# Performance work log

Measured on AMD Instinct MI355X. Metric: run time of the kernel, lower is better.

## Reference

```python
import jax, jax.numpy as jnp
import numpy as np

NT = 128          # num_timesteps (reference query points)
E = 128           # embed_time
H = 128           # nhidden
NH = 1            # num_heads
F = 32            # feature_size
NS = 2            # num_states
EPS = 1e-5


def layer_norm(x, g, b):
    m = jnp.mean(x, axis=-1, keepdims=True)
    v = jnp.mean((x - m) ** 2, axis=-1, keepdims=True)
    return (x - m) * jax.lax.rsqrt(v + EPS) * g + b


def setup_inputs() -> dict:
    key = jax.random.key(0)
    ks = jax.random.split(key, 24)
    nrm = lambda k, s: (jax.random.normal(k, s) * 0.05).astype(jnp.float32)
    inp = {
        "input": jax.random.normal(ks[0], (8, F, 512), dtype=jnp.float32),
        "mask": jax.random.randint(ks[1], (8, F, 512), 0, 2).astype(jnp.float32),
        "timesteps": jnp.sort(jax.random.uniform(ks[2], (8, 512), dtype=jnp.float32), axis=-1),
        # time embedding
        "periodic_w": nrm(ks[3], (E - 1, 1)), "periodic_b": nrm(ks[4], (E - 1,)),
        "lin_w": nrm(ks[5], (1, 1)), "lin_b": nrm(ks[6], (1,)),
        # query / key projections + layer norms
        "q_w": nrm(ks[7], (E, E)), "q_b": nrm(ks[8], (E,)),
        "q_g": jnp.ones((E,), jnp.float32), "q_be": jnp.zeros((E,), jnp.float32),
        "k_w": nrm(ks[9], (E, E)), "k_b": nrm(ks[10], (E,)),
        "k_g": jnp.ones((E,), jnp.float32), "k_be": jnp.zeros((E,), jnp.float32),
        # attention_norm over h*2F channels, then output linear + LN to nhidden
        "attn_g": jnp.ones((NH * 2 * F,), jnp.float32), "attn_b": jnp.zeros((NH * 2 * F,), jnp.float32),
        "out_w": nrm(ks[11], (H, NH * 2 * F)), "out_b": nrm(ks[12], (H,)),
        "out_g": jnp.ones((H,), jnp.float32), "out_be": jnp.zeros((H,), jnp.float32),
        # GRU (torch gate order r, z, n)
        "gru_wih": nrm(ks[13], (3 * H, H)), "gru_whh": nrm(ks[14], (3 * H, H)),
        "gru_bih": nrm(ks[15], (3 * H,)), "gru_bhh": nrm(ks[16], (3 * H,)),
        # classifier MLP
        "c1_w": nrm(ks[17], (H, H)), "c1_b": nrm(ks[18], (H,)),
        "c2_w": nrm(ks[19], (H, H)), "c2_b": nrm(ks[20], (H,)),
        "c3_w": nrm(ks[21], (NS, H)), "c3_b": nrm(ks[22], (NS,)),
    }
    return inp


def time_embedding(tt, lin_w, lin_b, periodic_w, periodic_b):
    t = tt[..., None]                                   # (..., 1)
    out1 = t @ lin_w.T + lin_b                          # (..., 1)
    out2 = jnp.sin(t @ periodic_w.T + periodic_b)       # (..., E-1)
    return jnp.concatenate([out1, out2], axis=-1)       # (..., E)


def reference(input, mask, timesteps, periodic_w, periodic_b, lin_w, lin_b,
              q_w, q_b, q_g, q_be, k_w, k_b, k_g, k_be,
              attn_g, attn_b, out_w, out_b, out_g, out_be,
              gru_wih, gru_whh, gru_bih, gru_bhh,
              c1_w, c1_b, c2_w, c2_b, c3_w, c3_b):
    B = input.shape[0]
    x_in = jnp.transpose(input, (0, 2, 1))              # (B, T, F)
    m = 1.0 - jnp.transpose(mask, (0, 2, 1))            # (B, T, F)
    x_in = x_in * (m > 0).astype(x_in.dtype)
    x = jnp.concatenate([x_in, m], axis=-1)             # (B, T, 2F)
    mk = jnp.concatenate([m, m], axis=-1)               # (B, T, 2F)

    key_e = time_embedding(timesteps, lin_w, lin_b, periodic_w, periodic_b)        # (B, T, E)
    qtimes = jnp.linspace(0.0, 1.0, NT)
    query_e = time_embedding(qtimes[None], lin_w, lin_b, periodic_w, periodic_b)   # (1, NT, E)

    q = layer_norm(query_e @ q_w.T + q_b, q_g, q_be)    # (1, NT, E)
    k = layer_norm(key_e @ k_w.T + k_b, k_g, k_be)      # (B, T, E)

    etk = E // NH
    q = q.reshape(1, NT, NH, etk).transpose(0, 2, 1, 3)         # (1, h, NT, etk)
    k = k.reshape(B, -1, NH, etk).transpose(0, 2, 1, 3)         # (B, h, T, etk)

    scores = jnp.einsum("ahqd,bhkd->bhqk", q, k) / np.sqrt(etk)  # (B, h, NT, T)
    # per-channel masked softmax over keys: (B, h, NT, T, 2F)
    logits = jnp.where(mk[:, None, None, :, :] == 0, -1e9, scores[..., None])
    p_attn = jax.nn.softmax(logits, axis=-2)
    att = jnp.sum(p_attn * x[:, None, None, :, :], axis=-2)     # (B, h, NT, 2F)

    x2 = att.transpose(0, 2, 1, 3).reshape(B, NT, NH * 2 * F)
    x2 = layer_norm(x2, attn_g, attn_b)
    out = layer_norm(x2 @ out_w.T + out_b, out_g, out_be)       # (B, NT, H)

    # GRU over the NT reference timesteps, last hidden state
    seq = out.transpose(1, 0, 2)                                # (NT, B, H)
    h0 = jnp.zeros((B, H), out.dtype)

    def gru_step(h, x_t):
        gi = x_t @ gru_wih.T + gru_bih
        gh = h @ gru_whh.T + gru_bhh
        ir, iz, inn = jnp.split(gi, 3, axis=-1)
        hr, hz, hn = jnp.split(gh, 3, axis=-1)
        r = jax.nn.sigmoid(ir + hr)
        z = jax.nn.sigmoid(iz + hz)
        n = jnp.tanh(inn + r * hn)
        h_new = (1.0 - z) * n + z * h
        return h_new, None

    h_last, _ = jax.lax.scan(gru_step, h0, seq)

    h1 = jax.nn.relu(h_last @ c1_w.T + c1_b)
    h2 = jax.nn.relu(h1 @ c2_w.T + c2_b)
    return h2 @ c3_w.T + c3_b                                   # (B, num_states) logits
```

## Files before the change

kernel.cpp:

```cpp
#include <hip/hip_runtime.h>
#include <math.h>

#define LN_EPS 1e-5f

typedef _Float16 h2v __attribute__((ext_vector_type(2)));

__device__ __forceinline__ float dot4(float4 a, float4 b) {
    return a.x*b.x + a.y*b.y + a.z*b.z + a.w*b.w;
}
__device__ __forceinline__ void fma4(float4& a, float s, float4 v) {
    a.x += s*v.x; a.y += s*v.y; a.z += s*v.z; a.w += s*v.w;
}
__device__ __forceinline__ float fast_rcp(float x) {
    return __builtin_amdgcn_rcpf(x);
}
__device__ __forceinline__ float fast_sigmoid(float x) {
    return fast_rcp(1.f + __expf(-x));
}
__device__ __forceinline__ float fast_tanh(float x) {
    return 1.f - 2.f*fast_rcp(__expf(2.f*x) + 1.f);
}
__device__ __forceinline__ float fdot2u(unsigned int a, unsigned int b, float c) {
#if __has_builtin(__builtin_amdgcn_fdot2)
    return __builtin_amdgcn_fdot2(__builtin_bit_cast(h2v, a),
                                  __builtin_bit_cast(h2v, b), c, false);
#else
    const h2v av = __builtin_bit_cast(h2v, a);
    const h2v bv = __builtin_bit_cast(h2v, b);
    return c + (float)av[0]*(float)bv[0] + (float)av[1]*(float)bv[1];
#endif
}
__device__ __forceinline__ float wsum64(float v) {
    #pragma unroll
    for (int off = 32; off > 0; off >>= 1) v += __shfl_xor(v, off);
    return v;
}

__global__ void k_embed_proj(
    const float* __restrict__ input, const float* __restrict__ mask,
    const float* __restrict__ timesteps,
    const float* __restrict__ pw, const float* __restrict__ pb,
    const float* __restrict__ lw, const float* __restrict__ lb,
    const float* __restrict__ q_w, const float* __restrict__ q_b,
    const float* __restrict__ q_g, const float* __restrict__ q_be,
    const float* __restrict__ k_w, const float* __restrict__ k_b,
    const float* __restrict__ k_g, const float* __restrict__ k_be,
    float* __restrict__ qs, float* __restrict__ kT, float2* __restrict__ xm)
{
    const int blk = blockIdx.x;
    const int tid = threadIdx.x;

    __shared__ __align__(16) float e[4][128];
    __shared__ __align__(16) float4 red[128];
    __shared__ __align__(16) float proj[4][128];
    __shared__ __align__(16) float2 tile[32][65];

    if (blk < 64) {
        const int b  = blk >> 3;
        const int t0 = (blk & 7) * 64;
        const int cg = tid >> 6;
        const int tt = tid & 63;
        #pragma unroll
        for (int c16 = 0; c16 < 16; ++c16) {
            const int c = c16*2 + cg;
            const float m = mask [(size_t)(b*32 + c)*512 + t0 + tt];
            const float x = input[(size_t)(b*32 + c)*512 + t0 + tt];
            const float mm = 1.0f - m;
            tile[c][tt] = make_float2(x*mm, mm);
        }
        __syncthreads();
        const int c2 = tid & 31;
        const int tg = tid >> 5;
        #pragma unroll
        for (int k = 0; k < 16; ++k) {
            const int t = tg*16 + k;
            xm[((size_t)b*512 + t0 + t)*32 + c2] = tile[c2][t];
        }
        return;
    }

    const bool isq = blk < 96;
    float tv[4];
    int kidx0 = 0;
    if (isq) {
        const int q0 = (blk - 64) * 4;
        #pragma unroll
        for (int r = 0; r < 4; ++r) tv[r] = (float)(q0 + r) * (1.0f/127.0f);
    } else {
        kidx0 = (blk - 96) * 4;
        #pragma unroll
        for (int r = 0; r < 4; ++r) tv[r] = timesteps[kidx0 + r];
    }

    float pwj = 0.f, pbj = 0.f;
    if (tid > 0) { pwj = pw[tid-1]; pbj = pb[tid-1]; }
    const float lw0 = lw[0], lb0 = lb[0];
    #pragma unroll
    for (int r = 0; r < 4; ++r)
        e[r][tid] = (tid == 0) ? (tv[r]*lw0 + lb0) : sinf(tv[r]*pwj + pbj);
    __syncthreads();

    const float* W  = isq ? q_w  : k_w;
    const float* Bv = isq ? q_b  : k_b;
    const float* G  = isq ? q_g  : k_g;
    const float* Be = isq ? q_be : k_be;

    {
        const int jj = tid >> 2, dc = tid & 3;
        const float4* e0 = (const float4*)(&e[0][0]);
        const float4* e1 = (const float4*)(&e[1][0]);
        const float4* e2 = (const float4*)(&e[2][0]);
        const float4* e3 = (const float4*)(&e[3][0]);
        #pragma unroll
        for (int jb = 0; jb < 4; ++jb) {
            const int j = jb*32 + jj;
            const float4* wrow = (const float4*)(W + (size_t)j*128);
            float a0=0.f, a1=0.f, a2=0.f, a3=0.f;
            #pragma unroll
            for (int k = 0; k < 8; ++k) {
                const int idx = dc + 4*k;
                const float4 w4 = wrow[idx];
                a0 += dot4(w4, e0[idx]);
                a1 += dot4(w4, e1[idx]);
                a2 += dot4(w4, e2[idx]);
                a3 += dot4(w4, e3[idx]);
            }
            a0 += __shfl_xor(a0, 1, 4); a0 += __shfl_xor(a0, 2, 4);
            a1 += __shfl_xor(a1, 1, 4); a1 += __shfl_xor(a1, 2, 4);
            a2 += __shfl_xor(a2, 1, 4); a2 += __shfl_xor(a2, 2, 4);
            a3 += __shfl_xor(a3, 1, 4); a3 += __shfl_xor(a3, 2, 4);
            if (dc == 0) {
                const float bj = Bv[j];
                proj[0][j] = a0 + bj; proj[1][j] = a1 + bj;
                proj[2][j] = a2 + bj; proj[3][j] = a3 + bj;
            }
        }
    }
    __syncthreads();

    float acc[4];
    #pragma unroll
    for (int r = 0; r < 4; ++r) acc[r] = proj[r][tid];

    red[tid] = make_float4(acc[0], acc[1], acc[2], acc[3]);
    __syncthreads();
    for (int s = 64; s > 0; s >>= 1) {
        if (tid < s) {
            float4 m = red[tid]; const float4 o = red[tid+s];
            m.x += o.x; m.y += o.y; m.z += o.z; m.w += o.w;
            red[tid] = m;
        }
        __syncthreads();
    }
    float4 mean = red[0];
    mean.x *= (1.0f/128.0f); mean.y *= (1.0f/128.0f);
    mean.z *= (1.0f/128.0f); mean.w *= (1.0f/128.0f);
    __syncthreads();
    const float d0 = acc[0]-mean.x, d1 = acc[1]-mean.y,
                d2 = acc[2]-mean.z, d3 = acc[3]-mean.w;
    red[tid] = make_float4(d0*d0, d1*d1, d2*d2, d3*d3);
    __syncthreads();
    for (int s = 64; s > 0; s >>= 1) {
        if (tid < s) {
            float4 m = red[tid]; const float4 o = red[tid+s];
            m.x += o.x; m.y += o.y; m.z += o.z; m.w += o.w;
            red[tid] = m;
        }
        __syncthreads();
    }
    float4 var = red[0];
    var.x *= (1.0f/128.0f); var.y *= (1.0f/128.0f);
    var.z *= (1.0f/128.0f); var.w *= (1.0f/128.0f);

    const float gg = G[tid], bb = Be[tid];
    const float o0 = d0*rsqrtf(var.x+LN_EPS)*gg + bb;
    const float o1 = d1*rsqrtf(var.y+LN_EPS)*gg + bb;
    const float o2 = d2*rsqrtf(var.z+LN_EPS)*gg + bb;
    const float o3 = d3*rsqrtf(var.w+LN_EPS)*gg + bb;

    if (isq) {
        const float sc = 0.08838834764831845f;
        const int q0 = (blk - 64)*4;
        qs[(size_t)(q0+0)*128 + tid] = o0*sc;
        qs[(size_t)(q0+1)*128 + tid] = o1*sc;
        qs[(size_t)(q0+2)*128 + tid] = o2*sc;
        qs[(size_t)(q0+3)*128 + tid] = o3*sc;
    } else {
        const int b = kidx0 >> 9;
        const int t = kidx0 & 511;
        *(float4*)(kT + ((size_t)(b*128 + tid))*512 + t) =
            make_float4(o0, o1, o2, o3);
    }
}

__global__ void __launch_bounds__(256) k_attn(
    const float2* __restrict__ xm,
    const float* __restrict__ qs, const float* __restrict__ kT,
    const float* __restrict__ attn_g, const float* __restrict__ attn_b,
    const float* __restrict__ out_w, const float* __restrict__ out_b,
    const float* __restrict__ out_g, const float* __restrict__ out_be,
    float* __restrict__ outm)
{
    const int b     = blockIdx.x >> 5;
    const int qbase = (blockIdx.x & 31) * 4;
    const int tid   = threadIdx.x;

    __shared__ __align__(16) float et[4][512];
    __shared__ __align__(16) float qsh[4][128];
    __shared__ __align__(16) float wsh[128*66];
    __shared__ __align__(16) float sA[4][8][32];
    __shared__ __align__(16) float aA[4][8][32];
    __shared__ __align__(16) float x2s[4][64];
    __shared__ float redC[4];

    for (int idx = tid; idx < 512; idx += 256)
        qsh[idx >> 7][idx & 127] = qs[(size_t)(qbase + (idx >> 7))*128 + (idx & 127)];
    for (int idx = tid; idx < 8192; idx += 256)
        wsh[(idx >> 6)*66 + (idx & 63)] = out_w[idx];
    __syncthreads();

    {
        const int grp = tid >> 7;
        const int tl  = tid & 127;
        const int q0  = grp*2;
        const float4* kp  = (const float4*)kT + (size_t)b*128*128 + tl;
        const float4* qa4 = (const float4*)qsh[q0];
        const float4* qb4 = (const float4*)qsh[q0+1];
        float4 a0 = make_float4(0,0,0,0), a1 = make_float4(0,0,0,0);
        float4 c0 = kp[0], c1 = kp[128], c2 = kp[256], c3 = kp[384];
        for (int c = 0; c < 32; ++c) {
            float4 n0, n1, n2, n3;
            if (c < 31) {
                const float4* kn = kp + (size_t)(4*c+4)*128;
                n0 = kn[0]; n1 = kn[128]; n2 = kn[256]; n3 = kn[384];
            }
            const float4 qa = qa4[c], qb = qb4[c];
            fma4(a0, qa.x, c0); fma4(a1, qb.x, c0);
            fma4(a0, qa.y, c1); fma4(a1, qb.y, c1);
            fma4(a0, qa.z, c2); fma4(a1, qb.z, c2);
            fma4(a0, qa.w, c3); fma4(a1, qb.w, c3);
            c0 = n0; c1 = n1; c2 = n2; c3 = n3;
        }
        a0.x = __expf(a0.x); a0.y = __expf(a0.y); a0.z = __expf(a0.z); a0.w = __expf(a0.w);
        a1.x = __expf(a1.x); a1.y = __expf(a1.y); a1.z = __expf(a1.z); a1.w = __expf(a1.w);
        ((float4*)et[q0])[tl]   = a0;
        ((float4*)et[q0+1])[tl] = a1;
    }
    __syncthreads();

    {
        const int c   = tid & 31;
        const int seg = tid >> 5;
        const float2* xp = xm + ((size_t)b*512 + seg*64)*32 + c;
        float s0=0,s1=0,s2=0,s3=0, a0=0,a1=0,a2=0,a3=0;
        #pragma unroll 4
        for (int i = 0; i < 64; ++i) {
            const float2 v = xp[(size_t)i*32];
            const int t = seg*64 + i;
            const float w0 = et[0][t]*v.y, w1 = et[1][t]*v.y;
            const float w2 = et[2][t]*v.y, w3 = et[3][t]*v.y;
            s0 += w0; s1 += w1; s2 += w2; s3 += w3;
            a0 += w0*v.x; a1 += w1*v.x; a2 += w2*v.x; a3 += w3*v.x;
        }
        sA[0][seg][c]=s0; sA[1][seg][c]=s1; sA[2][seg][c]=s2; sA[3][seg][c]=s3;
        aA[0][seg][c]=a0; aA[1][seg][c]=a1; aA[2][seg][c]=a2; aA[3][seg][c]=a3;
    }
    __syncthreads();

    {
        const int ql = tid >> 6;
        const int c2 = tid & 63;
        const int cc = c2 & 31;
        float ss = 0.f;
        #pragma unroll
        for (int g = 0; g < 8; ++g) ss += sA[ql][g][cc];
        float attv;
        if (c2 < 32) {
            float aa = 0.f;
            #pragma unroll
            for (int g = 0; g < 8; ++g) aa += aA[ql][g][cc];
            attv = (ss > 0.f) ? aa/ss : 0.f;
        } else {
            attv = (ss > 0.f) ? 1.0f : 0.0f;
        }
        const float mean = wsum64(attv) * (1.0f/64.0f);
        const float dv = attv - mean;
        const float var = wsum64(dv*dv) * (1.0f/64.0f);
        x2s[ql][c2] = dv*rsqrtf(var+LN_EPS)*attn_g[c2] + attn_b[c2];
    }
    __syncthreads();

    {
        const int jhalf = tid >> 7;
        const int j     = tid & 127;
        const int wave  = tid >> 6;
        for (int lq2 = 0; lq2 < 2; ++lq2) {
            const int ql = jhalf*2 + lq2;
            float acc = out_b[j];
            const float4* wrow = (const float4*)(wsh + j*66);
            const float4* xr   = (const float4*)x2s[ql];
            #pragma unroll
            for (int k = 0; k < 16; ++k) acc += dot4(wrow[k], xr[k]);

            float v = wsum64(acc);
            if ((tid & 63) == 0) redC[wave] = v;
            __syncthreads();
            const float mean = (redC[jhalf*2] + redC[jhalf*2+1]) * (1.0f/128.0f);
            __syncthreads();
            const float d = acc - mean;
            v = wsum64(d*d);
            if ((tid & 63) == 0) redC[wave] = v;
            __syncthreads();
            const float var = (redC[jhalf*2] + redC[jhalf*2+1]) * (1.0f/128.0f);
            outm[((size_t)b*128 + qbase + ql)*128 + j] =
                d*rsqrtf(var+LN_EPS)*out_g[j] + out_be[j];
            __syncthreads();
        }
    }
}

__global__ void k_gi(const float* __restrict__ outm,
                     const float* __restrict__ wih, const float* __restrict__ bih,
                     float* __restrict__ gi)
{
    const int qi  = blockIdx.x;
    const int tid = threadIdx.x;
    __shared__ __align__(16) float rows[8][128];
    for (int idx = tid; idx < 1024; idx += 384) {
        const int b = idx >> 7, d = idx & 127;
        rows[b][d] = outm[(size_t)(b*128+qi)*128 + d];
    }
    __syncthreads();

    const int g0 = tid >> 2, dc = tid & 3;
    #pragma unroll
    for (int gb = 0; gb < 4; ++gb) {
        const int g = gb*96 + g0;
        const float4* wrow = (const float4*)(wih + (size_t)g*128);
        float acc[8] = {0,0,0,0,0,0,0,0};
        #pragma unroll
        for (int k = 0; k < 8; ++k) {
            const int idx = dc + 4*k;
            const float4 w4 = wrow[idx];
            #pragma unroll
            for (int b = 0; b < 8; ++b)
                acc[b] += dot4(w4, ((const float4*)rows[b])[idx]);
        }
        #pragma unroll
        for (int b = 0; b < 8; ++b) {
            acc[b] += __shfl_xor(acc[b], 1, 4);
            acc[b] += __shfl_xor(acc[b], 2, 4);
        }
        if (dc == 0) {
            const float bi = bih[g];
            #pragma unroll
            for (int b = 0; b < 8; ++b)
                gi[((size_t)qi*8 + b)*384 + g] = acc[b] + bi;
        }
    }
}

__global__ void __launch_bounds__(512) k_gru_cls(
    const float* __restrict__ gi,
    const float* __restrict__ whh, const float* __restrict__ bhh,
    const float* __restrict__ c1w, const float* __restrict__ c1b,
    const float* __restrict__ c2w, const float* __restrict__ c2b,
    const float* __restrict__ c3w, const float* __restrict__ c3b,
    float* __restrict__ out)
{
    const int b   = blockIdx.x;
    const int tid = threadIdx.x;
    const int s   = tid >> 7;
    const int u   = tid & 127;

    __shared__ __align__(16) unsigned int lds[25344];
    unsigned int* hP = lds;
    float4* part4 = (float4*)&lds[64];
    float* hcls = (float*)&lds[64 + 1536];

    {
        const float4* w4 = (const float4*)whh;
        #pragma unroll 4
        for (int k = 0; k < 24; ++k) {
            const int idx = tid + k*512;
            const float4 v = w4[idx];
            const int row = idx >> 5, c4 = idx & 31;
            h2v p0; p0[0] = (_Float16)v.x; p0[1] = (_Float16)v.y;
            h2v p1; p1[0] = (_Float16)v.z; p1[1] = (_Float16)v.w;
            lds[row*66 + c4*2    ] = __builtin_bit_cast(unsigned int, p0);
            lds[row*66 + c4*2 + 1] = __builtin_bit_cast(unsigned int, p1);
        }
    }
    __syncthreads();

    unsigned int wreg[3][16];
    #pragma unroll
    for (int g = 0; g < 3; ++g) {
        const uint2* src = (const uint2*)&lds[(g*128 + u)*66 + 16*s];
        #pragma unroll
        for (int i = 0; i < 8; ++i) {
            const uint2 t = src[i];
            wreg[g][2*i] = t.x; wreg[g][2*i+1] = t.y;
        }
    }
    __syncthreads();

    const float* gbase = gi + (size_t)b*384;
    float bh_r=0.f, bh_z=0.f, bh_n=0.f, gr0=0.f, gz0=0.f, gn0=0.f, hprev=0.f;
    if (tid < 64) hP[tid] = 0u;
    if (s == 0) {
        bh_r = bhh[u]; bh_z = bhh[u+128]; bh_n = bhh[u+256];
        gr0 = gbase[u]; gz0 = gbase[u+128]; gn0 = gbase[u+256];
    }
    __syncthreads();

    for (int qi = 0; qi < 128; ++qi) {
        const uint4* hp4 = (const uint4*)hP + s*4;
        float ar = 0.f, az = 0.f, an = 0.f;
        #pragma unroll
        for (int i = 0; i < 4; ++i) {
            const uint4 hv = hp4[i];
            ar = fdot2u(wreg[0][4*i+0], hv.x, ar);
            ar = fdot2u(wreg[0][4*i+1], hv.y, ar);
            ar = fdot2u(wreg[0][4*i+2], hv.z, ar);
            ar = fdot2u(wreg[0][4*i+3], hv.w, ar);
            az = fdot2u(wreg[1][4*i+0], hv.x, az);
            az = fdot2u(wreg[1][4*i+1], hv.y, az);
            az = fdot2u(wreg[1][4*i+2], hv.z, az);
            az = fdot2u(wreg[1][4*i+3], hv.w, az);
            an = fdot2u(wreg[2][4*i+0], hv.x, an);
            an = fdot2u(wreg[2][4*i+1], hv.y, an);
            an = fdot2u(wreg[2][4*i+2], hv.z, an);
            an = fdot2u(wreg[2][4*i+3], hv.w, an);
        }
        if (s > 0) part4[(s-1)*128 + u] = make_float4(ar, az, an, 0.f);

        float grn=0.f, gzn=0.f, gnn=0.f;
        if (s == 0 && qi < 127) {
            const float* gb = gbase + (size_t)(qi+1)*3072;
            grn = gb[u]; gzn = gb[u+128]; gnn = gb[u+256];
        }
        __syncthreads();

        if (s == 0) {
            const float4 p0 = part4[u], p1 = part4[128+u], p2 = part4[256+u];
            const float ghr = ar + p0.x + p1.x + p2.x + bh_r;
            const float ghz = az + p0.y + p1.y + p2.y + bh_z;
            const float ghn = an + p0.z + p1.z + p2.z + bh_n;
            const float r = fast_sigmoid(gr0 + ghr);
            const float z = fast_sigmoid(gz0 + ghz);
            const float n = fast_tanh(gn0 + r*ghn);
            const float hn2 = (1.f - z)*n + z*hprev;
            hprev = hn2;
            gr0 = grn; gz0 = gzn; gn0 = gnn;
            const float other = __shfl_xor(hn2, 1);
            if ((u & 1) == 0) {
                h2v hp; hp[0] = (_Float16)hn2; hp[1] = (_Float16)other;
                hP[u >> 1] = __builtin_bit_cast(unsigned int, hp);
            }
        }
        __syncthreads();
    }

    float* scr = (float*)part4;
    if (s == 0) hcls[u] = hprev;
    __syncthreads();
    if (tid < 128) {
        float acc = c1b[u];
        const float4* wc = (const float4*)(c1w + (size_t)u*128);
        const float4* v  = (const float4*)hcls;
        #pragma unroll
        for (int d4 = 0; d4 < 32; ++d4) acc += dot4(wc[d4], v[d4]);
        scr[u] = fmaxf(acc, 0.f);
    }
    __syncthreads();
    if (tid < 128) {
        float acc = c2b[u];
        const float4* wc = (const float4*)(c2w + (size_t)u*128);
        const float4* v  = (const float4*)scr;
        #pragma unroll
        for (int d4 = 0; d4 < 32; ++d4) acc += dot4(wc[d4], v[d4]);
        scr[128 + u] = fmaxf(acc, 0.f);
    }
    __syncthreads();
    if (tid < 2) {
        float acc = c3b[tid];
        const float4* wc = (const float4*)(c3w + (size_t)tid*128);
        const float4* v  = (const float4*)(scr + 128);
        #pragma unroll
        for (int d4 = 0; d4 < 32; ++d4) acc += dot4(wc[d4], v[d4]);
        out[(size_t)b*2 + tid] = acc;
    }
}

extern "C" void kernel_launch(void* const* d_in, const int* in_sizes, int n_in,
                              void* d_out, int out_size, void* d_ws, size_t ws_size,
                              hipStream_t stream)
{
    const float* input     = (const float*)d_in[0];
    const float* mask      = (const float*)d_in[1];
    const float* timesteps = (const float*)d_in[2];
    const float* pw        = (const float*)d_in[3];
    const float* pb        = (const float*)d_in[4];
    const float* lw        = (const float*)d_in[5];
    const float* lb        = (const float*)d_in[6];
    const float* q_w       = (const float*)d_in[7];
    const float* q_b       = (const float*)d_in[8];
    const float* q_g       = (const float*)d_in[9];
    const float* q_be      = (const float*)d_in[10];
    const float* k_w       = (const float*)d_in[11];
    const float* k_b       = (const float*)d_in[12];
    const float* k_g       = (const float*)d_in[13];
    const float* k_be      = (const float*)d_in[14];
    const float* attn_g    = (const float*)d_in[15];
    const float* attn_b    = (const float*)d_in[16];
    const float* out_w     = (const float*)d_in[17];
    const float* out_b     = (const float*)d_in[18];
    const float* out_g     = (const float*)d_in[19];
    const float* out_be    = (const float*)d_in[20];
    const float* gru_wih   = (const float*)d_in[21];
    const float* gru_whh   = (const float*)d_in[22];
    const float* gru_bih   = (const float*)d_in[23];
    const float* gru_bhh   = (const float*)d_in[24];
    const float* c1_w      = (const float*)d_in[25];
    const float* c1_b      = (const float*)d_in[26];
    const float* c2_w      = (const float*)d_in[27];
    const float* c2_b      = (const float*)d_in[28];
    const float* c3_w      = (const float*)d_in[29];
    const float* c3_b      = (const float*)d_in[30];

    float* ws   = (float*)d_ws;
    float*  qs   = ws;
    float*  kT   = qs   + 16384;
    float*  outm = kT   + 524288;
    float*  gi   = outm + 131072;
    float2* xm   = (float2*)(gi + 393216);

    k_embed_proj<<<1120, 128, 0, stream>>>(input, mask, timesteps,
                                           pw, pb, lw, lb,
                                           q_w, q_b, q_g, q_be,
                                           k_w, k_b, k_g, k_be, qs, kT, xm);
    k_attn<<<256, 256, 0, stream>>>(xm, qs, kT,
                                    attn_g, attn_b, out_w, out_b,
                                    out_g, out_be, outm);
    k_gi<<<128, 384, 0, stream>>>(outm, gru_wih, gru_bih, gi);
    k_gru_cls<<<8, 512, 0, stream>>>(gi, gru_whh, gru_bhh,
                                     c1_w, c1_b, c2_w, c2_b, c3_w, c3_b,
                                     (float*)d_out);
}
```

Baseline: 240.5 us.

## Fuse all stages into one cooperative persistent kernel with grid syncs

Replaces the four separate kernel launches (embedding/projection, attention, GRU input projection, GRU+classifier) with a single cooperative kernel of 256 blocks of 512 threads. Grid-wide syncs separate the phases, and work items are remapped onto the persistent blocks. The outm buffer appears to be dropped, suggesting attention output now feeds the gi computation more directly. This removes launch gaps and inter-kernel drain, at the cost of grid sync overhead and a large shared-memory footprint per block.

```diff
diff --git a/kernel.cpp b/kernel.cpp
--- a/kernel.cpp
+++ b/kernel.cpp
@@ -1,5 +1,8 @@
 #include <hip/hip_runtime.h>
+#include <hip/hip_cooperative_groups.h>
 #include <math.h>
+
+namespace cg = cooperative_groups;
 
 #define LN_EPS 1e-5f
 
@@ -36,460 +39,461 @@
     return v;
 }
 
-__global__ void k_embed_proj(
-    const float* __restrict__ input, const float* __restrict__ mask,
-    const float* __restrict__ timesteps,
-    const float* __restrict__ pw, const float* __restrict__ pb,
-    const float* __restrict__ lw, const float* __restrict__ lb,
-    const float* __restrict__ q_w, const float* __restrict__ q_b,
-    const float* __restrict__ q_g, const float* __restrict__ q_be,
-    const float* __restrict__ k_w, const float* __restrict__ k_b,
-    const float* __restrict__ k_g, const float* __restrict__ k_be,
-    float* __restrict__ qs, float* __restrict__ kT, float2* __restrict__ xm)
+struct KP {
+    const float *input, *mask, *timesteps, *pw, *pb, *lw, *lb;
+    const float *q_w, *q_b, *q_g, *q_be, *k_w, *k_b, *k_g, *k_be;
+    const float *attn_g, *attn_b, *out_w, *out_b, *out_g, *out_be;
+    const float *wih, *whh, *bih, *bhh;
+    const float *c1w, *c1b, *c2w, *c2b, *c3w, *c3b;
+    float *qs, *kT, *gi;
+    float2 *xm;
+    float *out;
+};
+
+__global__ void __launch_bounds__(512) k_fused(KP p)
 {
+    __shared__ __align__(16) unsigned int lds[25344];
     const int blk = blockIdx.x;
     const int tid = threadIdx.x;
-
-    __shared__ __align__(16) float e[4][128];
-    __shared__ __align__(16) float4 red[128];
-    __shared__ __align__(16) float proj[4][128];
-    __shared__ __align__(16) float2 tile[32][65];
-
-    if (blk < 64) {
-        const int b  = blk >> 3;
-        const int t0 = (blk & 7) * 64;
-        const int cg = tid >> 6;
-        const int tt = tid & 63;
-        #pragma unroll
-        for (int c16 = 0; c16 < 16; ++c16) {
-            const int c = c16*2 + cg;
-            const float m = mask [(size_t)(b*32 + c)*512 + t0 + tt];
-            const float x = input[(size_t)(b*32 + c)*512 + t0 + tt];
-            const float mm = 1.0f - m;
-            tile[c][tt] = make_float2(x*mm, mm);
-        }
-        __syncthreads();
-        const int c2 = tid & 31;
-        const int tg = tid >> 5;
-        #pragma unroll
-        for (int k = 0; k < 16; ++k) {
-            const int t = tg*16 + k;
-            xm[((size_t)b*512 + t0 + t)*32 + c2] = tile[c2][t];
-        }
-        return;
+    cg::grid_group grid = cg::this_grid();
+
+    {
+        const int sg = tid >> 7;
+        const int t1 = tid & 127;
+        float*  e_    = (float*)lds;
+        float4* red4  = (float4*)((char*)lds + 8192);
+        float*  proj_ = (float*)((char*)lds + 16384);
+        float2* tile  = (float2*)lds;
+
+        for (int u = blk; u < 280; u += 256) {
+            if (u < 264) {
+                const bool isq = (u >= 256);
+                const int base = (isq ? (u - 256) : u) * 16 + sg * 4;
+                float tv[4];
+                #pragma unroll
+                for (int r = 0; r < 4; ++r)
+                    tv[r] = isq ? (float)(base + r) * (1.0f/127.0f)
+                                : p.timesteps[base + r];
+                float pwj = 0.f, pbj = 0.f;
+                if (t1 > 0) { pwj = p.pw[t1-1]; pbj = p.pb[t1-1]; }
+                const float lw0 = p.lw[0], lb0 = p.lb[0];
+                #pragma unroll
+                for (int r = 0; r < 4; ++r)
+                    e_[(sg*4 + r)*128 + t1] =
+                        (t1 == 0) ? (tv[r]*lw0 + lb0) : sinf(tv[r]*pwj + pbj);
+                __syncthreads();
+
+                const float* W  = isq ? p.q_w  : p.k_w;
+                const float* Bv = isq ? p.q_b  : p.k_b;
+                const float* G  = isq ? p.q_g  : p.k_g;
+                const float* Be = isq ? p.q_be : p.k_be;
+
+                {
+                    const int jj = t1 >> 2, dc = t1 & 3;
+                    const float4* e0 = (const float4*)(e_ + (sg*4+0)*128);
+                    const float4* e1 = (const float4*)(e_ + (sg*4+1)*128);
+                    const float4* e2 = (const float4*)(e_ + (sg*4+2)*128);
+                    const float4* e3 = (const float4*)(e_ + (sg*4+3)*128);
+                    #pragma unroll
+                    for (int jb = 0; jb < 4; ++jb) {
+                        const int j = jb*32 + jj;
+                        const float4* wrow = (const float4*)(W + (size_t)j*128);
+                        float a0=0.f, a1=0.f, a2=0.f, a3=0.f;
+                        #pragma unroll
+                        for (int k = 0; k < 8; ++k) {
+                            const int idx = dc + 4*k;
+                            const float4 w4 = wrow[idx];
+                            a0 += dot4(w4, e0[idx]);
+                            a1 += dot4(w4, e1[idx]);
+                            a2 += dot4(w4, e2[idx]);
+                            a3 += dot4(w4, e3[idx]);
+                        }
+                        a0 += __shfl_xor(a0, 1, 4); a0 += __shfl_xor(a0, 2, 4);
+                        a1 += __shfl_xor(a1, 1, 4); a1 += __shfl_xor(a1, 2, 4);
+                        a2 += __shfl_xor(a2, 1, 4); a2 += __shfl_xor(a2, 2, 4);
+                        a3 += __shfl_xor(a3, 1, 4); a3 += __shfl_xor(a3, 2, 4);
+                        if (dc == 0) {
+                            const float bj = Bv[j];
+                            proj_[(sg*4+0)*128 + j] = a0 + bj;
+                            proj_[(sg*4+1)*128 + j] = a1 + bj;
+                            proj_[(sg*4+2)*128 + j] = a2 + bj;
+                            proj_[(sg*4+3)*128 + j] = a3 + bj;
+                        }
+                    }
+                }
+                __syncthreads();
+
+                float acc[4];
+                #pragma unroll
+                for (int r = 0; r < 4; ++r) acc[r] = proj_[(sg*4+r)*128 + t1];
+
+                red4[sg*128 + t1] = make_float4(acc[0], acc[1], acc[2], acc[3]);
+                __syncthreads();
+                for (int s = 64; s > 0; s >>= 1) {
+                    if (t1 < s) {
+                        float4 m = red4[sg*128 + t1];
+                        const float4 o = red4[sg*128 + t1 + s];
+                        m.x += o.x; m.y += o.y; m.z += o.z; m.w += o.w;
+                        red4[sg*128 + t1] = m;
+                    }
+                    __syncthreads();
+                }
+                float4 mean = red4[sg*128];
+                mean.x *= (1.0f/128.0f); mean.y *= (1.0f/128.0f);
+                mean.z *= (1.0f/128.0f); mean.w *= (1.0f/128.0f);
+                __syncthreads();
+                const float d0 = acc[0]-mean.x, d1 = acc[1]-mean.y,
+                            d2 = acc[2]-mean.z, d3 = acc[3]-mean.w;
+                red4[sg*128 + t1] = make_float4(d0*d0, d1*d1, d2*d2, d3*d3);
+                __syncthreads();
+                for (int s = 64; s > 0; s >>= 1) {
+                    if (t1 < s) {
+                        float4 m = red4[sg*128 + t1];
+                        const float4 o = red4[sg*128 + t1 + s];
+                        m.x += o.x; m.y += o.y; m.z += o.z; m.w += o.w;
+                        red4[sg*128 + t1] = m;
+                    }
+                    __syncthreads();
+                }
+                float4 var = red4[sg*128];
+                var.x *= (1.0f/128.0f); var.y *= (1.0f/128.0f);
+                var.z *= (1.0f/128.0f); var.w *= (1.0f/128.0f);
+
+                const float gg = G[t1], bb = Be[t1];
+                const float o0 = d0*rsqrtf(var.x+LN_EPS)*gg + bb;
+                const float o1 = d1*rsqrtf(var.y+LN_EPS)*gg + bb;
+                const float o2 = d2*rsqrtf(var.z+LN_EPS)*gg + bb;
+                const float o3 = d3*rsqrtf(var.w+LN_EPS)*gg + bb;
+
+                if (isq) {
+                    const float sc = 0.08838834764831845f;
+                    p.qs[(size_t)(base+0)*128 + t1] = o0*sc;
+                    p.qs[(size_t)(base+1)*128 + t1] = o1*sc;
+                    p.qs[(size_t)(base+2)*128 + t1] = o2*sc;
+                    p.qs[(size_t)(base+3)*128 + t1] = o3*sc;
+                } else {
+                    const int b = base >> 9;
+                    const int t = base & 511;
+                    *(float4*)(p.kT + ((size_t)(b*128 + t1))*512 + t) =
+                        make_float4(o0, o1, o2, o3);
+                }
+            } else {
+                const int idx = u - 264;
+                const int b  = idx >> 1;
+                const int t0 = (idx & 1) * 256;
+                for (int k = tid; k < 8192; k += 512) {
+                    const int c = k >> 8, t = k & 255;
+                    const float m = p.mask [(size_t)(b*32 + c)*512 + t0 + t];
+                    const float x = p.input[(size_t)(b*32 + c)*512 + t0 + t];
+                    const float mm = 1.0f - m;
+                    tile[c*257 + t] = make_float2(x*mm, mm);
+                }
+                __syncthreads();
+                for (int k = tid; k < 8192; k += 512) {
+                    const int t = k >> 5, c = k & 31;
+                    p.xm[((size_t)b*512 + t0 + t)*32 + c] = tile[c*257 + t];
+                }
+            }
+            __syncthreads();
+        }
     }
-
-    const bool isq = blk < 96;
-    float tv[4];
-    int kidx0 = 0;
-    if (isq) {
-        const int q0 = (blk - 64) * 4;
-        #pragma unroll
-        for (int r = 0; r < 4; ++r) tv[r] = (float)(q0 + r) * (1.0f/127.0f);
-    } else {
-        kidx0 = (blk - 96) * 4;
-        #pragma unroll
-        for (int r = 0; r < 4; ++r) tv[r] = timesteps[kidx0 + r];
-    }
-
-    float pwj = 0.f, pbj = 0.f;
-    if (tid > 0) { pwj = pw[tid-1]; pbj = pb[tid-1]; }
-    const float lw0 = lw[0], lb0 = lb[0];
-    #pragma unroll
-    for (int r = 0; r < 4; ++r)
-        e[r][tid] = (tid == 0) ? (tv[r]*lw0 + lb0) : sinf(tv[r]*pwj + pbj);
-    __syncthreads();
-
-    const float* W  = isq ? q_w  : k_w;
-    const float* Bv = isq ? q_b  : k_b;
-    const float* G  = isq ? q_g  : k_g;
-    const float* Be = isq ? q_be : k_be;
+    __threadfence();
+    grid.sync();
 
     {
-        const int jj = tid >> 2, dc = tid & 3;
-        const float4* e0 = (const float4*)(&e[0][0]);
-        const float4* e1 = (const float4*)(&e[1][0]);
-        const float4* e2 = (const float4*)(&e[2][0]);
-        const float4* e3 = (const float4*)(&e[3][0]);
-        #pragma unroll
-        for (int jb = 0; jb < 4; ++jb) {
-            const int j = jb*32 + jj;
-            const float4* wrow = (const float4*)(W + (size_t)j*128);
-            float a0=0.f, a1=0.f, a2=0.f, a3=0.f;
-            #pragma unroll
-            for (int k = 0; k < 8; ++k) {
-                const int idx = dc + 4*k;
-                const float4 w4 = wrow[idx];
-                a0 += dot4(w4, e0[idx]);
-                a1 += dot4(w4, e1[idx]);
-                a2 += dot4(w4, e2[idx]);
-                a3 += dot4(w4, e3[idx]);
-            }
-            a0 += __shfl_xor(a0, 1, 4); a0 += __shfl_xor(a0, 2, 4);
-            a1 += __shfl_xor(a1, 1, 4); a1 += __shfl_xor(a1, 2, 4);
-            a2 += __shfl_xor(a2, 1, 4); a2 += __shfl_xor(a2, 2, 4);
-            a3 += __shfl_xor(a3, 1, 4); a3 += __shfl_xor(a3, 2, 4);
-            if (dc == 0) {
-                const float bj = Bv[j];
-                proj[0][j] = a0 + bj; proj[1][j] = a1 + bj;
-                proj[2][j] = a2 + bj; proj[3][j] = a3 + bj;
-            }
-        }
-    }
-    __syncthreads();
-
-    float acc[4];
-    #pragma unroll
-    for (int r = 0; r < 4; ++r) acc[r] = proj[r][tid];
-
-    red[tid] = make_float4(acc[0], acc[1], acc[2], acc[3]);
-    __syncthreads();
-    for (int s = 64; s > 0; s >>= 1) {
-        if (tid < s) {
-            float4 m = red[tid]; const float4 o = red[tid+s];
-            m.x += o.x; m.y += o.y; m.z += o.z; m.w += o.w;
-            red[tid] = m;
-        }
-        __syncthreads();
-    }
-    float4 mean = red[0];
-    mean.x *= (1.0f/128.0f); mean.y *= (1.0f/128.0f);
-    mean.z *= (1.0f/128.0f); mean.w *= (1.0f/128.0f);
-    __syncthreads();
-    const float d0 = acc[0]-mean.x, d1 = acc[1]-mean.y,
-                d2 = acc[2]-mean.z, d3 = acc[3]-mean.w;
-    red[tid] = make_float4(d0*d0, d1*d1, d2*d2, d3*d3);
-    __syncthreads();
-    for (int s = 64; s > 0; s >>= 1) {
-        if (tid < s) {
-            float4 m = red[tid]; const float4 o = red[tid+s];
-            m.x += o.x; m.y += o.y; m.z += o.z; m.w += o.w;
-            red[tid] = m;
-        }
-        __syncthreads();
-    }
-    float4 var = red[0];
-    var.x *= (1.0f/128.0f); var.y *= (1.0f/128.0f);
-    var.z *= (1.0f/128.0f); var.w *= (1.0f/128.0f);
-
-    const float gg = G[tid], bb = Be[tid];
-    const float o0 = d0*rsqrtf(var.x+LN_EPS)*gg + bb;
-    const float o1 = d1*rsqrtf(var.y+LN_EPS)*gg + bb;
-    const float o2 = d2*rsqrtf(var.z+LN_EPS)*gg + bb;
-    const float o3 = d3*rsqrtf(var.w+LN_EPS)*gg + bb;
-
-    if (isq) {
-        const float sc = 0.08838834764831845f;
-        const int q0 = (blk - 64)*4;
-        qs[(size_t)(q0+0)*128 + tid] = o0*sc;
-        qs[(size_t)(q0+1)*128 + tid] = o1*sc;
-        qs[(size_t)(q0+2)*128 + tid] = o2*sc;
-        qs[(size_t)(q0+3)*128 + tid] = o3*sc;
-    } else {
-        const int b = kidx0 >> 9;
-        const int t = kidx0 & 511;
-        *(float4*)(kT + ((size_t)(b*128 + tid))*512 + t) =
-            make_float4(o0, o1, o2, o3);
-    }
-}
-
-__global__ void __launch_bounds__(256) k_attn(
-    const float2* __restrict__ xm,
-    const float* __restrict__ qs, const float* __restrict__ kT,
-    const float* __restrict__ attn_g, const float* __restrict__ attn_b,
-    const float* __restrict__ out_w, const float* __restrict__ out_b,
-    const float* __restrict__ out_g, const float* __restrict__ out_be,
-    float* __restrict__ outm)
-{
-    const int b     = blockIdx.x >> 5;
-    const int qbase = (blockIdx.x & 31) * 4;
-    const int tid   = threadIdx.x;
-
-    __shared__ __align__(16) float et[4][512];
-    __shared__ __align__(16) float qsh[4][128];
-    __shared__ __align__(16) float wsh[128*66];
-    __shared__ __align__(16) float sA[4][8][32];
-    __shared__ __align__(16) float aA[4][8][32];
-    __shared__ __align__(16) float x2s[4][64];
-    __shared__ float redC[4];
-
-    for (int idx = tid; idx < 512; idx += 256)
-        qsh[idx >> 7][idx & 127] = qs[(size_t)(qbase + (idx >> 7))*128 + (idx & 127)];
-    for (int idx = tid; idx < 8192; idx += 256)
-        wsh[(idx >> 6)*66 + (idx & 63)] = out_w[idx];
-    __syncthreads();
-
-    {
-        const int grp = tid >> 7;
-        const int tl  = tid & 127;
-        const int q0  = grp*2;
-        const float4* kp  = (const float4*)kT + (size_t)b*128*128 + tl;
-        const float4* qa4 = (const float4*)qsh[q0];
-        const float4* qb4 = (const float4*)qsh[q0+1];
-        float4 a0 = make_float4(0,0,0,0), a1 = make_float4(0,0,0,0);
-        float4 c0 = kp[0], c1 = kp[128], c2 = kp[256], c3 = kp[384];
-        for (int c = 0; c < 32; ++c) {
-            float4 n0, n1, n2, n3;
-            if (c < 31) {
-                const float4* kn = kp + (size_t)(4*c+4)*128;
-                n0 = kn[0]; n1 = kn[128]; n2 = kn[256]; n3 = kn[384];
-            }
-            const float4 qa = qa4[c], qb = qb4[c];
-            fma4(a0, qa.x, c0); fma4(a1, qb.x, c0);
-            fma4(a0, qa.y, c1); fma4(a1, qb.y, c1);
-            fma4(a0, qa.z, c2); fma4(a1, qb.z, c2);
-            fma4(a0, qa.w, c3); fma4(a1, qb.w, c3);
-            c0 = n0; c1 = n1; c2 = n2; c3 = n3;
-        }
-        a0.x = __expf(a0.x); a0.y = __expf(a0.y); a0.z = __expf(a0.z); a0.w = __expf(a0.w);
-        a1.x = __expf(a1.x); a1.y = __expf(a1.y); a1.z = __expf(a1.z); a1.w = __expf(a1.w);
-        ((float4*)et[q0])[tl]   = a0;
-        ((float4*)et[q0+1])[tl] = a1;
-    }
-    __syncthreads();
-
-    {
-        const int c   = tid & 31;
-        const int seg = tid >> 5;
-        const float2* xp = xm + ((size_t)b*512 + seg*64)*32 + c;
-        float s0=0,s1=0,s2=0,s3=0, a0=0,a1=0,a2=0,a3=0;
-        #pragma unroll 4
-        for (int i = 0; i < 64; ++i) {
-            const float2 v = xp[(size_t)i*32];
-            const int t = seg*64 + i;
-            const float w0 = et[0][t]*v.y, w1 = et[1][t]*v.y;
-            const float w2 = et[2][t]*v.y, w3 = et[3][t]*v.y;
-            s0 += w0; s1 += w1; s2 += w2; s3 += w3;
-            a0 += w0*v.x; a1 += w1*v.x; a2 += w2*v.x; a3 += w3*v.x;
-        }
-        sA[0][seg][c]=s0; sA[1][seg][c]=s1; sA[2][seg][c]=s2; sA[3][seg][c]=s3;
-        aA[0][seg][c]=a0; aA[1][seg][c]=a1; aA[2][seg][c]=a2; aA[3][seg][c]=a3;
-    }
-    __syncthreads();
-
-    {
-        const int ql = tid >> 6;
-        const int c2 = tid & 63;
-        const int cc = c2 & 31;
-        float ss = 0.f;
-        #pragma unroll
-        for (int g = 0; g < 8; ++g) ss += sA[ql][g][cc];
-        float attv;
-        if (c2 < 32) {
-            float aa = 0.f;
-            #pragma unroll
-            for (int g = 0; g < 8; ++g) aa += aA[ql][g][cc];
-            attv = (ss > 0.f) ? aa/ss : 0.f;
-        } else {
-            attv = (ss > 0.f) ? 1.0f : 0.0f;
-        }
-        const float mean = wsum64(attv) * (1.0f/64.0f);
-        const float dv = attv - mean;
-        const float var = wsum64(dv*dv) * (1.0f/64.0f);
-        x2s[ql][c2] = dv*rsqrtf(var+LN_EPS)*attn_g[c2] + attn_b[c2];
-    }
-    __syncthreads();
-
-    {
-        const int jhalf = tid >> 7;
-        const int j     = tid & 127;
-        const int wave  = tid >> 6;
-        for (int lq2 = 0; lq2 < 2; ++lq2) {
-            const int ql = jhalf*2 + lq2;
-            float acc = out_b[j];
-            const float4* wrow = (const float4*)(wsh + j*66);
-            const float4* xr   = (const float4*)x2s[ql];
+        const int b     = blk >> 5;
+        const int qbase = (blk & 31) * 4;
+
+        char* lmem = (char*)lds;
+        float4* et4    = (float4*)lmem;
+        float*  qshf   = (float*)(lmem + 8192);
+        float*  wshf   = (float*)(lmem + 10240);
+        float4* part4  = (float4*)(lmem + 44032);
+        float*  sAf    = (float*)(lmem + 76800);
+        float*  aAf    = (float*)(lmem + 84992);
+        float*  x2sf   = (float*)(lmem + 93184);
+        float*  rows4f = (float*)(lmem + 94208);
+        float*  redC   = (float*)(lmem + 96256);
+        float*  redD   = (float*)(lmem + 96288);
+
+        qshf[tid] = p.qs[(size_t)qbase*128 + tid];
+        for (int idx = tid; idx < 8192; idx += 512)
+            wshf[(idx >> 6)*66 + (idx & 63)] = p.out_w[idx];
+        __syncthreads();
+
+        {
+            const int grp = tid >> 7;
+            const int tl  = tid & 127;
+            const float4* kp  = (const float4*)p.kT
+                                + ((size_t)(b*128 + grp*32))*128 + tl;
+            const float4* q0 = (const float4*)(qshf +   0) + grp*8;
+            const float4* q1 = (const float4*)(qshf + 128) + grp*8;
+            const float4* q2 = (const float4*)(qshf + 256) + grp*8;
+            const float4* q3 = (const float4*)(qshf + 384) + grp*8;
+            float4 a0 = make_float4(0,0,0,0), a1 = a0, a2 = a0, a3 = a0;
+            float4 c0 = kp[0], c1 = kp[128], c2 = kp[256], c3 = kp[384];
+            for (int c = 0; c < 8; ++c) {
+                float4 n0, n1, n2, n3;
+                if (c < 7) {
+                    const float4* kn = kp + (size_t)(4*c+4)*128;
+                    n0 = kn[0]; n1 = kn[128]; n2 = kn[256]; n3 = kn[384];
+                }
+                const float4 qa = q0[c], qb = q1[c], qc = q2[c], qd = q3[c];
+                fma4(a0, qa.x, c0); fma4(a1, qb.x, c0); fma4(a2, qc.x, c0); fma4(a3, qd.x, c0);
+                fma4(a0, qa.y, c1); fma4(a1, qb.y, c1); fma4(a2, qc.y, c1); fma4(a3, qd.y, c1);
+                fma4(a0, qa.z, c2); fma4(a1, qb.z, c2); fma4(a2, qc.z, c2); fma4(a3, qd.z, c2);
+                fma4(a0, qa.w, c3); fma4(a1, qb.w, c3); fma4(a2, qc.w, c3); fma4(a3, qd.w, c3);
+                c0 = n0; c1 = n1; c2 = n2; c3 = n3;
+            }
+            part4[(grp*4 + 0)*128 + tl] = a0;
+            part4[(grp*4 + 1)*128 + tl] = a1;
+            part4[(grp*4 + 2)*128 + tl] = a2;
+            part4[(grp*4 + 3)*128 + tl] = a3;
+        }
+        __syncthreads();
+
+        {
+            const int t = tid;
+            const int tl4 = t >> 2, cm = t & 3;
+            const float* pf = (const float*)part4;
+            float v[4];
+            #pragma unroll
+            for (int ql = 0; ql < 4; ++ql) {
+                float s = 0.f;
+                #pragma unroll
+                for (int g = 0; g < 4; ++g)
+                    s += pf[((g*4 + ql)*128 + tl4)*4 + cm];
+                v[ql] = __expf(s);
+            }
+            et4[t] = make_float4(v[0], v[1], v[2], v[3]);
+        }
+        __syncthreads();
+
+        {
+            const int c   = tid & 31;
+            const int seg = tid >> 5;
+            const float2* xp = p.xm + ((size_t)b*512 + seg*32)*32 + c;
+            float s0=0,s1=0,s2=0,s3=0, a0=0,a1=0,a2=0,a3=0;
+            #pragma unroll 4
+            for (int i = 0; i < 32; ++i) {
+                const float2 v = xp[(size_t)i*32];
+                const float4 e = et4[seg*32 + i];
+                const float w0 = e.x*v.y, w1 = e.y*v.y, w2 = e.z*v.y, w3 = e.w*v.y;
+                s0 += w0; s1 += w1; s2 += w2; s3 += w3;
+                a0 += w0*v.x; a1 += w1*v.x; a2 += w2*v.x; a3 += w3*v.x;
+            }
+            sAf[(0*16 + seg)*32 + c] = s0; aAf[(0*16 + seg)*32 + c] = a0;
+            sAf[(1*16 + seg)*32 + c] = s1; aAf[(1*16 + seg)*32 + c] = a1;
+            sAf[(2*16 + seg)*32 + c] = s2; aAf[(2*16 + seg)*32 + c] = a2;
+            sAf[(3*16 + seg)*32 + c] = s3; aAf[(3*16 + seg)*32 + c] = a3;
+        }
+        __syncthreads();
+
+        if (tid < 256) {
+            const int ql = tid >> 6;
+            const int c2 = tid & 63;
+            const int cc = c2 & 31;
+            float ss = 0.f;
+            #pragma unroll
+            for (int g = 0; g < 16; ++g) ss += sAf[(ql*16 + g)*32 + cc];
+            float attv;
+            if (c2 < 32) {
+                float aa = 0.f;
+                #pragma unroll
+                for (int g = 0; g < 16; ++g) aa += aAf[(ql*16 + g)*32 + cc];
+                attv = (ss > 0.f) ? aa/ss : 0.f;
+            } else {
+                attv = (ss > 0.f) ? 1.0f : 0.0f;
+            }
+            const float mean = wsum64(attv) * (1.0f/64.0f);
+            const float dv = attv - mean;
+            const float var = wsum64(dv*dv) * (1.0f/64.0f);
+            x2sf[ql*64 + c2] = dv*rsqrtf(var+LN_EPS)*p.attn_g[c2] + p.attn_b[c2];
+        }
+        __syncthreads();
+
+        {
+            const int ql = tid >> 7;
+            const int j  = tid & 127;
+            const int w  = tid >> 6;
+            float acc = p.out_b[j];
+            const float4* wrow = (const float4*)(wshf + j*66);
+            const float4* xr   = (const float4*)(x2sf + ql*64);
             #pragma unroll
             for (int k = 0; k < 16; ++k) acc += dot4(wrow[k], xr[k]);
 
             float v = wsum64(acc);
-            if ((tid & 63) == 0) redC[wave] = v;
+            if ((tid & 63) == 0) redC[w] = v;
             __syncthreads();
-            const float mean = (redC[jhalf*2] + redC[jhalf*2+1]) * (1.0f/128.0f);
-            __syncthreads();
+            const float mean = (redC[ql*2] + redC[ql*2+1]) * (1.0f/128.0f);
             const float d = acc - mean;
             v = wsum64(d*d);
-            if ((tid & 63) == 0) redC[wave] = v;
+            if ((tid & 63) == 0) redD[w] = v;
             __syncthreads();
-            const float var = (redC[jhalf*2] + redC[jhalf*2+1]) * (1.0f/128.0f);
-            outm[((size_t)b*128 + qbase + ql)*128 + j] =
-                d*rsqrtf(var+LN_EPS)*out_g[j] + out_be[j];
+            const float var = (redD[ql*2] + redD[ql*2+1]) * (1.0f/128.0f);
+            rows4f[ql*128 + j] =
+                d*rsqrtf(var+LN_EPS)*p.out_g[j] + p.out_be[j];
+        }
+        __syncthreads();
+
+        {
+            const float4* rows44 = (const float4*)rows4f;
+            const int dc = tid & 3;
+            #pragma unroll
+            for (int pass = 0; pass < 3; ++pass) {
+                const int g = pass*128 + (tid >> 2);
+                const float4* wrow = (const float4*)(p.wih + (size_t)g*128);
+                float ac0=0.f, ac1=0.f, ac2=0.f, ac3=0.f;
+                #pragma unroll
+                for (int k = 0; k < 8; ++k) {
+                    const int idx = dc + 4*k;
+                    const float4 w4 = wrow[idx];
+                    ac0 += dot4(w4, rows44[0*32 + idx]);
+                    ac1 += dot4(w4, rows44[1*32 + idx]);
+                    ac2 += dot4(w4, rows44[2*32 + idx]);
+                    ac3 += dot4(w4, rows44[3*32 + idx]);
+                }
+                ac0 += __shfl_xor(ac0, 1, 4); ac0 += __shfl_xor(ac0, 2, 4);
+                ac1 += __shfl_xor(ac1, 1, 4); ac1 += __shfl_xor(ac1, 2, 4);
+                ac2 += __shfl_xor(ac2, 1, 4); ac2 += __shfl_xor(ac2, 2, 4);
+                ac3 += __shfl_xor(ac3, 1, 4); ac3 += __shfl_xor(ac3, 2, 4);
+                if (dc == 0) {
+                    const float bg = p.bih[g];
+                    p.gi[((size_t)(qbase+0)*8 + b)*384 + g] = ac0 + bg;
+                    p.gi[((size_t)(qbase+1)*8 + b)*384 + g] = ac1 + bg;
+                    p.gi[((size_t)(qbase+2)*8 + b)*384 + g] = ac2 + bg;
+                    p.gi[((size_t)(qbase+3)*8 + b)*384 + g] = ac3 + bg;
+                }
+            }
+        }
+    }
+    __threadfence();
+    grid.sync();
+
+    if (blk >= 8) return;
+
+    {
+        const int b = blk;
+        const int s = tid >> 7;
+        const int u = tid & 127;
+
+        unsigned int* hP = lds;
+        float4* partg = (float4*)&lds[64];
+        float*  hcls  = (float*)&lds[64 + 1536];
+
+        {
+            const float4* w4 = (const float4*)p.whh;
+            #pragma unroll 4
+            for (int k = 0; k < 24; ++k) {
+                const int idx = tid + k*512;
+                const float4 v = w4[idx];
+                const int row = idx >> 5, c4 = idx & 31;
+                h2v p0; p0[0] = (_Float16)v.x; p0[1] = (_Float16)v.y;
+                h2v p1; p1[0] = (_Float16)v.z; p1[1] = (_Float16)v.w;
+                lds[row*66 + c4*2    ] = __builtin_bit_cast(unsigned int, p0);
+                lds[row*66 + c4*2 + 1] = __builtin_bit_cast(unsigned int, p1);
+            }
+        }
+        __syncthreads();
+
+        unsigned int wreg[3][16];
+        #pragma unroll
+        for (int g = 0; g < 3; ++g) {
+            const uint2* src = (const uint2*)&lds[(g*128 + u)*66 + 16*s];
+            #pragma unroll
+            for (int i = 0; i < 8; ++i) {
+                const uint2 t = src[i];
+                wreg[g][2*i] = t.x; wreg[g][2*i+1] = t.y;
+            }
+        }
+        __syncthreads();
+
+        const float* gbase = p.gi + (size_t)b*384;
+        float bh_r=0.f, bh_z=0.f, bh_n=0.f, gr0=0.f, gz0=0.f, gn0=0.f, hprev=0.f;
+        if (tid < 64) hP[tid] = 0u;
+        if (s == 0) {
+            bh_r = p.bhh[u]; bh_z = p.bhh[u+128]; bh_n = p.bhh[u+256];
+            gr0 = gbase[u]; gz0 = gbase[u+128]; gn0 = gbase[u+256];
+        }
+        __syncthreads();
+
+        for (int qi = 0; qi < 128; ++qi) {
+            const uint4* hp4 = (const uint4*)hP + s*4;
+            float ar = 0.f, az = 0.f, an = 0.f;
+            #pragma unroll
+            for (int i = 0; i < 4; ++i) {
+                const uint4 hv = hp4[i];
+                ar = fdot2u(wreg[0][4*i+0], hv.x, ar);
+                ar = fdot2u(wreg[0][4*i+1], hv.y, ar);
+                ar = fdot2u(wreg[0][4*i+2], hv.z, ar);
+                ar = fdot2u(wreg[0][4*i+3], hv.w, ar);
+                az = fdot2u(wreg[1][4*i+0], hv.x, az);
+                az = fdot2u(wreg[1][4*i+1], hv.y, az);
+                az = fdot2u(wreg[1][4*i+2], hv.z, az);
+                az = fdot2u(wreg[1][4*i+3], hv.w, az);
+                an = fdot2u(wreg[2][4*i+0], hv.x, an);
+                an = fdot2u(wreg[2][4*i+1], hv.y, an);
+                an = fdot2u(wreg[2][4*i+2], hv.z, an);
+                an = fdot2u(wreg[2][4*i+3], hv.w, an);
+            }
+            if (s > 0) partg[(s-1)*128 + u] = make_float4(ar, az, an, 0.f);
+
+            float grn=0.f, gzn=0.f, gnn=0.f;
+            if (s == 0 && qi < 127) {
+                const float* gb = gbase + (size_t)(qi+1)*3072;
+                grn = gb[u]; gzn = gb[u+128]; gnn = gb[u+256];
+            }
             __syncthreads();
-        }
-    }
-}
-
-__global__ void k_gi(const float* __restrict__ outm,
-                     const float* __restrict__ wih, const float* __restrict__ bih,
-                     float* __restrict__ gi)
-{
-    const int qi  = blockIdx.x;
-    const int tid = threadIdx.x;
-    __shared__ __align__(16) float rows[8][128];
-    for (int idx = tid; idx < 1024; idx += 384) {
-        const int b = idx >> 7, d = idx & 127;
-        rows[b][d] = outm[(size_t)(b*128+qi)*128 + d];
-    }
-    __syncthreads();
-
-    const int g0 = tid >> 2, dc = tid & 3;
-    #pragma unroll
-    for (int gb = 0; gb < 4; ++gb) {
-        const int g = gb*96 + g0;
-        const float4* wrow = (const float4*)(wih + (size_t)g*128);
-        float acc[8] = {0,0,0,0,0,0,0,0};
-        #pragma unroll
-        for (int k = 0; k < 8; ++k) {
-            const int idx = dc + 4*k;
-            const float4 w4 = wrow[idx];
-            #pragma unroll
-            for (int b = 0; b < 8; ++b)
-                acc[b] += dot4(w4, ((const float4*)rows[b])[idx]);
-        }
-        #pragma unroll
-        for (int b = 0; b < 8; ++b) {
-            acc[b] += __shfl_xor(acc[b], 1, 4);
-            acc[b] += __shfl_xor(acc[b], 2, 4);
-        }
-        if (dc == 0) {
-            const float bi = bih[g];
-            #pragma unroll
-            for (int b = 0; b < 8; ++b)
-                gi[((size_t)qi*8 + b)*384 + g] = acc[b] + bi;
-        }
-    }
-}
-
-__global__ void __launch_bounds__(512) k_gru_cls(
-    const float* __restrict__ gi,
-    const float* __restrict__ whh, const float* __restrict__ bhh,
-    const float* __restrict__ c1w, const float* __restrict__ c1b,
-    const float* __restrict__ c2w, const float* __restrict__ c2b,
-    const float* __restrict__ c3w, const float* __restrict__ c3b,
-    float* __restrict__ out)
-{
-    const int b   = blockIdx.x;
-    const int tid = threadIdx.x;
-    const int s   = tid >> 7;
-    const int u   = tid & 127;
-
-    __shared__ __align__(16) unsigned int lds[25344];
-    unsigned int* hP = lds;
-    float4* part4 = (float4*)&lds[64];
-    float* hcls = (float*)&lds[64 + 1536];
-
-    {
-        const float4* w4 = (const float4*)whh;
-        #pragma unroll 4
-        for (int k = 0; k < 24; ++k) {
-            const int idx = tid + k*512;
-            const float4 v = w4[idx];
-            const int row = idx >> 5, c4 = idx & 31;
-            h2v p0; p0[0] = (_Float16)v.x; p0[1] = (_Float16)v.y;
-            h2v p1; p1[0] = (_Float16)v.z; p1[1] = (_Float16)v.w;
-            lds[row*66 + c4*2    ] = __builtin_bit_cast(unsigned int, p0);
-            lds[row*66 + c4*2 + 1] = __builtin_bit_cast(unsigned int, p1);
-        }
-    }
-    __syncthreads();
-
-    unsigned int wreg[3][16];
-    #pragma unroll
-    for (int g = 0; g < 3; ++g) {
-        const uint2* src = (const uint2*)&lds[(g*128 + u)*66 + 16*s];
-        #pragma unroll
-        for (int i = 0; i < 8; ++i) {
-            const uint2 t = src[i];
-            wreg[g][2*i] = t.x; wreg[g][2*i+1] = t.y;
-        }
-    }
-    __syncthreads();
-
-    const float* gbase = gi + (size_t)b*384;
-    float bh_r=0.f, bh_z=0.f, bh_n=0.f, gr0=0.f, gz0=0.f, gn0=0.f, hprev=0.f;
-    if (tid < 64) hP[tid] = 0u;
-    if (s == 0) {
-        bh_r = bhh[u]; bh_z = bhh[u+128]; bh_n = bhh[u+256];
-        gr0 = gbase[u]; gz0 = gbase[u+128]; gn0 = gbase[u+256];
-    }
-    __syncthreads();
-
-    for (int qi = 0; qi < 128; ++qi) {
-        const uint4* hp4 = (const uint4*)hP + s*4;
-        float ar = 0.f, az = 0.f, an = 0.f;
-        #pragma unroll
-        for (int i = 0; i < 4; ++i) {
-            const uint4 hv = hp4[i];
-            ar = fdot2u(wreg[0][4*i+0], hv.x, ar);
-            ar = fdot2u(wreg[0][4*i+1], hv.y, ar);
-            ar = fdot2u(wreg[0][4*i+2], hv.z, ar);
-            ar = fdot2u(wreg[0][4*i+3], hv.w, ar);
-            az = fdot2u(wreg[1][4*i+0], hv.x, az);
-            az = fdot2u(wreg[1][4*i+1], hv.y, az);
-            az = fdot2u(wreg[1][4*i+2], hv.z, az);
-            az = fdot2u(wreg[1][4*i+3], hv.w, az);
-            an = fdot2u(wreg[2][4*i+0], hv.x, an);
-            an = fdot2u(wreg[2][4*i+1], hv.y, an);
-            an = fdot2u(wreg[2][4*i+2], hv.z, an);
-            an = fdot2u(wreg[2][4*i+3], hv.w, an);
-        }
-        if (s > 0) part4[(s-1)*128 + u] = make_float4(ar, az, an, 0.f);
-
-        float grn=0.f, gzn=0.f, gnn=0.f;
-        if (s == 0 && qi < 127) {
-            const float* gb = gbase + (size_t)(qi+1)*3072;
-            grn = gb[u]; gzn = gb[u+128]; gnn = gb[u+256];
-        }
-        __syncthreads();
-
-        if (s == 0) {
-            const float4 p0 = part4[u], p1 = part4[128+u], p2 = part4[256+u];
-            const float ghr = ar + p0.x + p1.x + p2.x + bh_r;
-            const float ghz = az + p0.y + p1.y + p2.y + bh_z;
-            const float ghn = an + p0.z + p1.z + p2.z + bh_n;
-            const float r = fast_sigmoid(gr0 + ghr);
-            const float z = fast_sigmoid(gz0 + ghz);
-            const float n = fast_tanh(gn0 + r*ghn);
-            const float hn2 = (1.f - z)*n + z*hprev;
-            hprev = hn2;
-            gr0 = grn; gz0 = gzn; gn0 = gnn;
-            const float other = __shfl_xor(hn2, 1);
-            if ((u & 1) == 0) {
-                h2v hp; hp[0] = (_Float16)hn2; hp[1] = (_Float16)other;
-                hP[u >> 1] = __builtin_bit_cast(unsigned int, hp);
-            }
-        }
-        __syncthreads();
-    }
-
-    float* scr = (float*)part4;
-    if (s == 0) hcls[u] = hprev;
-    __syncthreads();
-    if (tid < 128) {
-        float acc = c1b[u];
-        const float4* wc = (const float4*)(c1w + (size_t)u*128);
-        const float4* v  = (const float4*)hcls;
-        #pragma unroll
-        for (int d4 = 0; d4 < 32; ++d4) acc += dot4(wc[d4], v[d4]);
-        scr[u] = fmaxf(acc, 0.f);
-    }
-    __syncthreads();
-    if (tid < 128) {
-        float acc = c2b[u];
-        const float4* wc = (const float4*)(c2w + (size_t)u*128);
-        const float4* v  = (const float4*)scr;
-        #pragma unroll
-        for (int d4 = 0; d4 < 32; ++d4) acc += dot4(wc[d4], v[d4]);
-        scr[128 + u] = fmaxf(acc, 0.f);
-    }
-    __syncthreads();
-    if (tid < 2) {
-        float acc = c3b[tid];
-        const float4* wc = (const float4*)(c3w + (size_t)tid*128);
-        const float4* v  = (const float4*)(scr + 128);
-        #pragma unroll
-        for (int d4 = 0; d4 < 32; ++d4) acc += dot4(wc[d4], v[d4]);
-        out[(size_t)b*2 + tid] = acc;
+
+            if (s == 0) {
+                const float4 p0 = partg[u], p1 = partg[128+u], p2 = partg[256+u];
+                const float ghr = ar + p0.x + p1.x + p2.x + bh_r;
+                const float ghz = az + p0.y + p1.y + p2.y + bh_z;
+                const float ghn = an + p0.z + p1.z + p2.z + bh_n;
+                const float r = fast_sigmoid(gr0 + ghr);
+                const float z = fast_sigmoid(gz0 + ghz);
+                const float n = fast_tanh(gn0 + r*ghn);
+                const float hn2 = (1.f - z)*n + z*hprev;
+                hprev = hn2;
+                gr0 = grn; gz0 = gzn; gn0 = gnn;
+                const float other = __shfl_xor(hn2, 1);
+                if ((u & 1) == 0) {
+                    h2v hp; hp[0] = (_Float16)hn2; hp[1] = (_Float16)other;
+                    hP[u >> 1] = __builtin_bit_cast(unsigned int, hp);
+                }
+            }
+            __syncthreads();
+        }
+
+        float* scr = (float*)partg;
+        if (s == 0) hcls[u] = hprev;
+        __syncthreads();
+        if (tid < 128) {
+            float acc = p.c1b[u];
+            const float4* wc = (const float4*)(p.c1w + (size_t)u*128);
+            const float4* v  = (const float4*)hcls;
+            #pragma unroll
+            for (int d4 = 0; d4 < 32; ++d4) acc += dot4(wc[d4], v[d4]);
+            scr[u] = fmaxf(acc, 0.f);
+        }
+        __syncthreads();
+        if (tid < 128) {
+            float acc = p.c2b[u];
+            const float4* wc = (const float4*)(p.c2w + (size_t)u*128);
+            const float4* v  = (const float4*)scr;
+            #pragma unroll
+            for (int d4 = 0; d4 < 32; ++d4) acc += dot4(wc[d4], v[d4]);
+            scr[128 + u] = fmaxf(acc, 0.f);
+        }
+        __syncthreads();
+        if (tid < 2) {
+            float acc = p.c3b[tid];
+            const float4* wc = (const float4*)(p.c3w + (size_t)tid*128);
+            const float4* v  = (const float4*)(scr + 128);
+            #pragma unroll
+            for (int d4 = 0; d4 < 32; ++d4) acc += dot4(wc[d4], v[d4]);
+            p.out[(size_t)b*2 + tid] = acc;
+        }
     }
 }
 
@@ -497,54 +501,47 @@
                               void* d_out, int out_size, void* d_ws, size_t ws_size,
                               hipStream_t stream)
 {
-    const float* input     = (const float*)d_in[0];
-    const float* mask      = (const float*)d_in[1];
-    const float* timesteps = (const float*)d_in[2];
-    const float* pw        = (const float*)d_in[3];
-    const float* pb        = (const float*)d_in[4];
-    const float* lw        = (const float*)d_in[5];
-    const float* lb        = (const float*)d_in[6];
-    const float* q_w       = (const float*)d_in[7];
-    const float* q_b       = (const float*)d_in[8];
-    const float* q_g       = (const float*)d_in[9];
-    const float* q_be      = (const float*)d_in[10];
-    const float* k_w       = (const float*)d_in[11];
-    const float* k_b       = (const float*)d_in[12];
-    const float* k_g       = (const float*)d_in[13];
-    const float* k_be      = (const float*)d_in[14];
-    const float* attn_g    = (const float*)d_in[15];
-    const float* attn_b    = (const float*)d_in[16];
-    const float* out_w     = (const float*)d_in[17];
-    const float* out_b     = (const float*)d_in[18];
-    const float* out_g     = (const float*)d_in[19];
-    const float* out_be    = (const float*)d_in[20];
-    const float* gru_wih   = (const float*)d_in[21];
-    const float* gru_whh   = (const float*)d_in[22];
-    const float* gru_bih   = (const float*)d_in[23];
-    const float* gru_bhh   = (const float*)d_in[24];
-    const float* c1_w      = (const float*)d_in[25];
-    const float* c1_b      = (const float*)d_in[26];
-    const float* c2_w      = (const float*)d_in[27];
-    const float* c2_b      = (const float*)d_in[28];
-    const float* c3_w      = (const float*)d_in[29];
-    const float* c3_b      = (const float*)d_in[30];
-
-    float* ws   = (float*)d_ws;
-    float*  qs   = ws;
-    float*  kT   = qs   + 16384;
-    float*  outm = kT   + 524288;
-    float*  gi   = outm + 131072;
-    float2* xm   = (float2*)(gi + 393216);
-
-    k_embed_proj<<<1120, 128, 0, stream>>>(input, mask, timesteps,
-                                           pw, pb, lw, lb,
-                                           q_w, q_b, q_g, q_be,
-                                           k_w, k_b, k_g, k_be, qs, kT, xm);
-    k_attn<<<256, 256, 0, stream>>>(xm, qs, kT,
-                                    attn_g, attn_b, out_w, out_b,
-                                    out_g, out_be, outm);
-    k_gi<<<128, 384, 0, stream>>>(outm, gru_wih, gru_bih, gi);
-    k_gru_cls<<<8, 512, 0, stream>>>(gi, gru_whh, gru_bhh,
-                                     c1_w, c1_b, c2_w, c2_b, c3_w, c3_b,
-                                     (float*)d_out);
-}
+    float* ws = (float*)d_ws;
+    KP p;
+    p.input     = (const float*)d_in[0];
+    p.mask      = (const float*)d_in[1];
+    p.timesteps = (const float*)d_in[2];
+    p.pw        = (const float*)d_in[3];
+    p.pb        = (const float*)d_in[4];
+    p.lw        = (const float*)d_in[5];
+    p.lb        = (const float*)d_in[6];
+    p.q_w       = (const float*)d_in[7];
+    p.q_b       = (const float*)d_in[8];
+    p.q_g       = (const float*)d_in[9];
+    p.q_be      = (const float*)d_in[10];
+    p.k_w       = (const float*)d_in[11];
+    p.k_b       = (const float*)d_in[12];
+    p.k_g       = (const float*)d_in[13];
+    p.k_be      = (const float*)d_in[14];
+    p.attn_g    = (const float*)d_in[15];
+    p.attn_b    = (const float*)d_in[16];
+    p.out_w     = (const float*)d_in[17];
+    p.out_b     = (const float*)d_in[18];
+    p.out_g     = (const float*)d_in[19];
+    p.out_be    = (const float*)d_in[20];
+    p.wih       = (const float*)d_in[21];
+    p.whh       = (const float*)d_in[22];
+    p.bih       = (const float*)d_in[23];
+    p.bhh       = (const float*)d_in[24];
+    p.c1w       = (const float*)d_in[25];
+    p.c1b       = (const float*)d_in[26];
+    p.c2w       = (const float*)d_in[27];
+    p.c2b       = (const float*)d_in[28];
+    p.c3w       = (const float*)d_in[29];
+    p.c3b       = (const float*)d_in[30];
+
+    p.qs  = ws;
+    p.kT  = ws + 16384;
+    p.gi  = ws + 16384 + 524288;
+    p.xm  = (float2*)(ws + 16384 + 524288 + 393216);
+    p.out = (float*)d_out;
+
+    void* args[] = { &p };
+    hipLaunchCooperativeKernel((void*)k_fused, dim3(256), dim3(512),
+                               args, 0, stream);
+}
```

After: 423.3 us. 1.76x slower.
